# Kernel optimization log

Hardware: AMD Instinct MI355X
Metric: run time of the kernel (lower is better)

## Reference

```python
import jax, jax.numpy as jnp
import numpy as np

STEPS = 200
DECAY = 0.5
VTH = 0.5


def setup_inputs() -> dict:
    key = jax.random.key(0)
    x = jax.random.normal(key, (32, 8192, STEPS), dtype=jnp.float32)
    return {"x": x}


def reference(x):
    # LIF forward (output=False path): sequential scan over the last (time) axis.
    # u = decay*u + i - o_prev*Vth ; o = heaviside(u - Vth)
    xt = jnp.moveaxis(x, -1, 0)  # [steps, batch, neurons]

    def step(carry, i):
        u, o = carry
        u = DECAY * u + i - o * VTH
        o = (u - VTH > 0).astype(x.dtype)
        return (u, o), o

    u0 = jnp.zeros(x.shape[:-1], dtype=x.dtype)
    o0 = jnp.zeros(x.shape[:-1], dtype=x.dtype)
    _, out_t = jax.lax.scan(step, (u0, o0), xt)
    return jnp.moveaxis(out_t, 0, -1)  # [batch, neurons, steps]
```

## Files before the change

kernel.cpp:

```cpp
#include <hip/hip_runtime.h>
#include <stdint.h>


#define STEPS 200
#define TPB 128

typedef __attribute__((address_space(3))) uint32_t lds_u32;
typedef __attribute__((address_space(1))) const uint32_t glb_u32;
typedef __attribute__((ext_vector_type(4))) float f32x4;

#define WAITV(n) do { asm volatile("s_waitcnt vmcnt(" #n ")" ::: "memory"); \
                      __builtin_amdgcn_sched_barrier(0); } while (0)

__device__ __forceinline__ void lif1(float xi, float& u, float& d,
                                     uint32_t& m, uint32_t bit) {
    float t = __fmaf_rn(0.5f, u, xi);
    u = __fsub_rn(t, d);
    bool sp = (u > 0.5f);
    d = sp ? 0.5f : 0.0f;
    m |= sp ? bit : 0u;
}

__device__ __forceinline__ void stage16(const float* __restrict__ src_base,
                                        float4* buf, int t0) {
#pragma unroll
    for (int i = 0; i < 4; ++i)
        __builtin_amdgcn_global_load_lds((const glb_u32*)(src_base + i * 16 * STEPS + t0),
                                         (lds_u32*)(buf + i * 64), 16, 0, 0);
}

__device__ __forceinline__ void stage8(const float* __restrict__ srcT,
                                       float4* buf) {
#pragma unroll
    for (int i = 0; i < 2; ++i)
        __builtin_amdgcn_global_load_lds((const glb_u32*)(srcT + i * 32 * STEPS),
                                         (lds_u32*)(buf + i * 64), 16, 0, 0);
}

__device__ __forceinline__ uint32_t scan16(const float4* buf, int lane,
                                           float& u, float& d) {
    const int sw = (lane >> 1) & 3;
    float4 rx[4];
#pragma unroll
    for (int c = 0; c < 4; ++c)
        rx[c] = buf[lane * 4 + (c ^ sw)];
    uint32_t m = 0;
#pragma unroll
    for (int g = 0; g < 4; ++g) {
        lif1(rx[g].x, u, d, m, 1u << (4 * g + 0));
        lif1(rx[g].y, u, d, m, 1u << (4 * g + 1));
        lif1(rx[g].z, u, d, m, 1u << (4 * g + 2));
        lif1(rx[g].w, u, d, m, 1u << (4 * g + 3));
    }
    return m;
}

__device__ __forceinline__ uint32_t scan8(const float4* buf, int lane,
                                          float& u, float& d) {
    float4 r0 = buf[lane * 2 + 0];
    float4 r1 = buf[lane * 2 + 1];
    uint32_t m = 0;
    lif1(r0.x, u, d, m, 1u);   lif1(r0.y, u, d, m, 2u);
    lif1(r0.z, u, d, m, 4u);   lif1(r0.w, u, d, m, 8u);
    lif1(r1.x, u, d, m, 16u);  lif1(r1.y, u, d, m, 32u);
    lif1(r1.z, u, d, m, 64u);  lif1(r1.w, u, d, m, 128u);
    return m;
}

__global__ __launch_bounds__(TPB) void lif_kernel(const float* __restrict__ x,
                                                  float* __restrict__ out)
{
    __shared__ float4 tile[2 * 4 * 256];
    const int tid = threadIdx.x;
    const int w = tid >> 6, lane = tid & 63;
    const long long wrow0 = (long long)blockIdx.x * TPB + w * 64;
    const float* xb = x + wrow0 * STEPS;
    float4* B[4] = { tile + w * 1024,        tile + w * 1024 + 256,
                     tile + w * 1024 + 512,  tile + w * 1024 + 768 };

    const float* srcS = xb + (lane >> 2) * STEPS + (((lane & 3) ^ ((lane >> 3) & 3)) << 2);
    const float* srcT = xb + (lane >> 1) * STEPS + ((lane & 1) << 2) + 192;

    float u = 0.0f, d = 0.0f;
    uint32_t w0, w1, w2, w3, w4, w5, w6;

    stage16(srcS, B[0], 0);
    stage16(srcS, B[1], 16);
    stage16(srcS, B[2], 32);

    stage16(srcS, B[3], 48);   WAITV(12); w0  = scan16(B[0], lane, u, d);
    stage16(srcS, B[0], 64);   WAITV(12); w0 |= scan16(B[1], lane, u, d) << 16;
    stage16(srcS, B[1], 80);   WAITV(12); w1  = scan16(B[2], lane, u, d);
    stage16(srcS, B[2], 96);   WAITV(12); w1 |= scan16(B[3], lane, u, d) << 16;
    stage16(srcS, B[3], 112);  WAITV(12); w2  = scan16(B[0], lane, u, d);
    stage16(srcS, B[0], 128);  WAITV(12); w2 |= scan16(B[1], lane, u, d) << 16;
    stage16(srcS, B[1], 144);  WAITV(12); w3  = scan16(B[2], lane, u, d);
    stage16(srcS, B[2], 160);  WAITV(12); w3 |= scan16(B[3], lane, u, d) << 16;
    stage16(srcS, B[3], 176);  WAITV(12); w4  = scan16(B[0], lane, u, d);
    stage8(srcT, B[0]);        WAITV(10); w4 |= scan16(B[1], lane, u, d) << 16;
                               WAITV(6);  w5  = scan16(B[2], lane, u, d);
                               WAITV(2);  w5 |= scan16(B[3], lane, u, d) << 16;
                               WAITV(0);  w6  = scan8(B[0], lane, u, d);

    uint32_t* bits = reinterpret_cast<uint32_t*>(B[1]);
    bits[lane * 8 + 0] = w0; bits[lane * 8 + 1] = w1; bits[lane * 8 + 2] = w2;
    bits[lane * 8 + 3] = w3; bits[lane * 8 + 4] = w4; bits[lane * 8 + 5] = w5;
    bits[lane * 8 + 6] = w6;

    float* ob = out + wrow0 * STEPS;
#pragma unroll
    for (int s = 0; s < 50; ++s) {
        int f = s * 64 + lane;
        int r = f / 50;
        int c = f - r * 50;
        uint32_t wd = bits[r * 8 + (c >> 3)] >> (((c >> 2) & 1) * 16 + (c & 3) * 4);
        f32x4 v;
        v.x = (wd & 1u) ? 1.0f : 0.0f;
        v.y = (wd & 2u) ? 1.0f : 0.0f;
        v.z = (wd & 4u) ? 1.0f : 0.0f;
        v.w = (wd & 8u) ? 1.0f : 0.0f;
        __builtin_nontemporal_store(v, reinterpret_cast<f32x4*>(ob + f * 4));
    }
}

extern "C" void kernel_launch(void* const* d_in, const int* in_sizes, int n_in,
                              void* d_out, int out_size, void* d_ws, size_t ws_size,
                              hipStream_t stream)
{
    const float* x = (const float*)d_in[0];
    float* out = (float*)d_out;
    int nrows = in_sizes[0] / STEPS;
    int grid = nrows / TPB;
    lif_kernel<<<grid, TPB, 0, stream>>>(x, out);
}
```

Before: 73.90 us.

## Interleave output stores with the scan pipeline instead of storing at the end

Output spikes are now written in 32-step bursts right after each pair of scan chunks, using a small per-wave LDS word buffer. Before, all 200 steps were written in one tail loop after the scan. The goal is to overlap write traffic with the remaining input loads and compute. Because stores also count toward vmcnt, the wait counts are retuned to match. This trades long contiguous row writes for 128-byte segments per row and adds extra LDS round-trips per burst. There is also a risk from reusing the LDS buffer without a wave barrier, and miscounted waits could stall or break correctness.

Result: slower. 136.4 us (+84.6%).

```diff
diff --git a/kernel.cpp b/kernel.cpp
--- a/kernel.cpp
+++ b/kernel.cpp
@@ -67,60 +67,85 @@
     return m;
 }
 
+__device__ __forceinline__ void store_burst(float* __restrict__ ob,
+                                            uint32_t* bw, int lane,
+                                            int t0, uint32_t word) {
+    bw[lane] = word;
+#pragma unroll
+    for (int i = 0; i < 8; ++i) {
+        int f = i * 64 + lane;
+        int r = f >> 3, c = f & 7;
+        uint32_t wd = bw[r] >> (c * 4);
+        f32x4 v;
+        v.x = (wd & 1u) ? 1.0f : 0.0f;
+        v.y = (wd & 2u) ? 1.0f : 0.0f;
+        v.z = (wd & 4u) ? 1.0f : 0.0f;
+        v.w = (wd & 8u) ? 1.0f : 0.0f;
+        __builtin_nontemporal_store(v, reinterpret_cast<f32x4*>(ob + r * STEPS + t0 + c * 4));
+    }
+}
+
+__device__ __forceinline__ void store_tail(float* __restrict__ ob,
+                                           uint32_t* bw, int lane, uint32_t word) {
+    bw[lane] = word;
+#pragma unroll
+    for (int s = 0; s < 2; ++s) {
+        int f = s * 64 + lane;
+        int r = f >> 1, c = f & 1;
+        uint32_t wd = bw[r] >> (c * 4);
+        f32x4 v;
+        v.x = (wd & 1u) ? 1.0f : 0.0f;
+        v.y = (wd & 2u) ? 1.0f : 0.0f;
+        v.z = (wd & 4u) ? 1.0f : 0.0f;
+        v.w = (wd & 8u) ? 1.0f : 0.0f;
+        __builtin_nontemporal_store(v, reinterpret_cast<f32x4*>(ob + r * STEPS + 192 + c * 4));
+    }
+}
+
 __global__ __launch_bounds__(TPB) void lif_kernel(const float* __restrict__ x,
                                                   float* __restrict__ out)
 {
     __shared__ float4 tile[2 * 4 * 256];
+    __shared__ uint32_t bword[2][64];
     const int tid = threadIdx.x;
     const int w = tid >> 6, lane = tid & 63;
     const long long wrow0 = (long long)blockIdx.x * TPB + w * 64;
     const float* xb = x + wrow0 * STEPS;
+    float* ob = out + wrow0 * STEPS;
     float4* B[4] = { tile + w * 1024,        tile + w * 1024 + 256,
                      tile + w * 1024 + 512,  tile + w * 1024 + 768 };
+    uint32_t* bw = bword[w];
 
     const float* srcS = xb + (lane >> 2) * STEPS + (((lane & 3) ^ ((lane >> 3) & 3)) << 2);
     const float* srcT = xb + (lane >> 1) * STEPS + ((lane & 1) << 2) + 192;
 
     float u = 0.0f, d = 0.0f;
-    uint32_t w0, w1, w2, w3, w4, w5, w6;
+    uint32_t lo, wd;
 
     stage16(srcS, B[0], 0);
     stage16(srcS, B[1], 16);
     stage16(srcS, B[2], 32);
 
-    stage16(srcS, B[3], 48);   WAITV(12); w0  = scan16(B[0], lane, u, d);
-    stage16(srcS, B[0], 64);   WAITV(12); w0 |= scan16(B[1], lane, u, d) << 16;
-    stage16(srcS, B[1], 80);   WAITV(12); w1  = scan16(B[2], lane, u, d);
-    stage16(srcS, B[2], 96);   WAITV(12); w1 |= scan16(B[3], lane, u, d) << 16;
-    stage16(srcS, B[3], 112);  WAITV(12); w2  = scan16(B[0], lane, u, d);
-    stage16(srcS, B[0], 128);  WAITV(12); w2 |= scan16(B[1], lane, u, d) << 16;
-    stage16(srcS, B[1], 144);  WAITV(12); w3  = scan16(B[2], lane, u, d);
-    stage16(srcS, B[2], 160);  WAITV(12); w3 |= scan16(B[3], lane, u, d) << 16;
-    stage16(srcS, B[3], 176);  WAITV(12); w4  = scan16(B[0], lane, u, d);
-    stage8(srcT, B[0]);        WAITV(10); w4 |= scan16(B[1], lane, u, d) << 16;
-                               WAITV(6);  w5  = scan16(B[2], lane, u, d);
-                               WAITV(2);  w5 |= scan16(B[3], lane, u, d) << 16;
-                               WAITV(0);  w6  = scan8(B[0], lane, u, d);
-
-    uint32_t* bits = reinterpret_cast<uint32_t*>(B[1]);
-    bits[lane * 8 + 0] = w0; bits[lane * 8 + 1] = w1; bits[lane * 8 + 2] = w2;
-    bits[lane * 8 + 3] = w3; bits[lane * 8 + 4] = w4; bits[lane * 8 + 5] = w5;
-    bits[lane * 8 + 6] = w6;
-
-    float* ob = out + wrow0 * STEPS;
-#pragma unroll
-    for (int s = 0; s < 50; ++s) {
-        int f = s * 64 + lane;
-        int r = f / 50;
-        int c = f - r * 50;
-        uint32_t wd = bits[r * 8 + (c >> 3)] >> (((c >> 2) & 1) * 16 + (c & 3) * 4);
-        f32x4 v;
-        v.x = (wd & 1u) ? 1.0f : 0.0f;
-        v.y = (wd & 2u) ? 1.0f : 0.0f;
-        v.z = (wd & 4u) ? 1.0f : 0.0f;
-        v.w = (wd & 8u) ? 1.0f : 0.0f;
-        __builtin_nontemporal_store(v, reinterpret_cast<f32x4*>(ob + f * 4));
-    }
+    stage16(srcS, B[3], 48);   WAITV(12); lo = scan16(B[0], lane, u, d);
+    stage16(srcS, B[0], 64);   WAITV(12); wd = lo | (scan16(B[1], lane, u, d) << 16);
+    store_burst(ob, bw, lane, 0, wd);
+    stage16(srcS, B[1], 80);   WAITV(20); lo = scan16(B[2], lane, u, d);
+    stage16(srcS, B[2], 96);   WAITV(20); wd = lo | (scan16(B[3], lane, u, d) << 16);
+    store_burst(ob, bw, lane, 32, wd);
+    stage16(srcS, B[3], 112);  WAITV(28); lo = scan16(B[0], lane, u, d);
+    stage16(srcS, B[0], 128);  WAITV(20); wd = lo | (scan16(B[1], lane, u, d) << 16);
+    store_burst(ob, bw, lane, 64, wd);
+    stage16(srcS, B[1], 144);  WAITV(28); lo = scan16(B[2], lane, u, d);
+    stage16(srcS, B[2], 160);  WAITV(20); wd = lo | (scan16(B[3], lane, u, d) << 16);
+    store_burst(ob, bw, lane, 96, wd);
+    stage16(srcS, B[3], 176);  WAITV(28); lo = scan16(B[0], lane, u, d);
+    stage8(srcT, B[0]);        WAITV(18); wd = lo | (scan16(B[1], lane, u, d) << 16);
+    store_burst(ob, bw, lane, 128, wd);
+                               WAITV(22); lo = scan16(B[2], lane, u, d);
+                               WAITV(10); wd = lo | (scan16(B[3], lane, u, d) << 16);
+    store_burst(ob, bw, lane, 160, wd);
+                               WAITV(16); wd = scan8(B[0], lane, u, d);
+    store_tail(ob, bw, lane, wd);
 }
 
 extern "C" void kernel_launch(void* const* d_in, const int* in_sizes, int n_in,
```
